# Optimization experiments

Hardware: AMD Instinct MI355X
Metric: run time of the kernel (lower is better)

## Reference

```python
import jax, jax.numpy as jnp
import numpy as np

B, S, DIM = 1, 2048, 4096
N_HEADS, N_KV_HEADS = 32, 8
HEAD_DIM = DIM // N_HEADS            # 128
N_REP = N_HEADS // N_KV_HEADS        # 4
Q_SIZE = N_HEADS * HEAD_DIM          # 4096
KV_SIZE = N_KV_HEADS * HEAD_DIM      # 1024


def setup_inputs() -> dict:
    key = jax.random.key(0)
    ks = jax.random.split(key, 5)
    x = jax.random.normal(ks[0], (B, S, DIM), dtype=jnp.float32)
    # RoPE tables: freqs_cis[s, j] = exp(i * s * theta_j), theta_j = 10000^(-2j/head_dim)
    theta = 10000.0 ** (-jnp.arange(0, HEAD_DIM, 2, dtype=jnp.float32) / HEAD_DIM)
    ang = jnp.arange(S, dtype=jnp.float32)[:, None] * theta[None, :]  # [S, HEAD_DIM//2]
    freqs_cos = jnp.cos(ang)
    freqs_sin = jnp.sin(ang)
    # causal additive mask [1,1,S,S]
    causal = jnp.tril(jnp.ones((S, S), dtype=bool))
    mask = jnp.where(causal, 0.0, -1e9).astype(jnp.float32)[None, None]
    wqkv = jax.random.normal(ks[1], (Q_SIZE + 2 * KV_SIZE, DIM), dtype=jnp.float32) * (DIM ** -0.5)
    wo = jax.random.normal(ks[2], (DIM, Q_SIZE), dtype=jnp.float32) * (Q_SIZE ** -0.5)
    return {"x": x, "freqs_cos": freqs_cos, "freqs_sin": freqs_sin, "mask": mask,
            "wqkv": wqkv, "wo": wo}


def _apply_rope(t, cos, sin):
    # t: [B, S, H, D]; cos/sin: [S, D//2]  (complex multiply on (even, odd) pairs)
    b, s, h, d = t.shape
    tp = t.reshape(b, s, h, d // 2, 2)
    t0, t1 = tp[..., 0], tp[..., 1]
    c = cos[None, :, None, :]
    sn = sin[None, :, None, :]
    out = jnp.stack([t0 * c - t1 * sn, t0 * sn + t1 * c], axis=-1)
    return out.reshape(b, s, h, d)


def reference(x, freqs_cos, freqs_sin, mask, wqkv, wo):
    bsz, seqlen, _ = x.shape
    qkv = jnp.einsum('bsd,od->bso', x, wqkv)  # fused QKV projection
    xq = qkv[..., :Q_SIZE].reshape(bsz, seqlen, N_HEADS, HEAD_DIM)
    xk = qkv[..., Q_SIZE:Q_SIZE + KV_SIZE].reshape(bsz, seqlen, N_KV_HEADS, HEAD_DIM)
    xv = qkv[..., Q_SIZE + KV_SIZE:].reshape(bsz, seqlen, N_KV_HEADS, HEAD_DIM)
    # rotary embedding on q, k
    xq = _apply_rope(xq, freqs_cos, freqs_sin)
    xk = _apply_rope(xk, freqs_cos, freqs_sin)
    # cache insertion (prefill: cache == current k/v), layout [B, KVH, S, D]
    cache_k = jnp.swapaxes(xk, 1, 2)
    cache_v = jnp.swapaxes(xv, 1, 2)
    # GQA repeat_kv -> [B, H, S, D]
    keys = jnp.repeat(cache_k, N_REP, axis=1)
    values = jnp.repeat(cache_v, N_REP, axis=1)
    # scores: einsum 'ijkl,ikml->ikjm' with xq [b,s,h,d], keys [b,h,t,d] -> [b,h,s,t]
    scores = jnp.einsum('bshd,bhtd->bhst', xq, keys) / jnp.sqrt(jnp.float32(HEAD_DIM))
    scores = scores + mask
    scores = jax.nn.softmax(scores.astype(jnp.float32), axis=-1).astype(xq.dtype)
    out = jnp.einsum('bhst,bhtd->bhsd', scores, values)  # [B, H, S, D]
    out = jnp.swapaxes(out, 1, 2).reshape(bsz, seqlen, Q_SIZE)
    return jnp.einsum('bso,do->bsd', out, wo)
```

## Files before the change

### kernel.cpp

```cpp
#include <hip/hip_runtime.h>
#include <hip/hip_bf16.h>
#include <cstdint>
#include <cstddef>


typedef __attribute__((ext_vector_type(4)))  float    f32x4;
typedef __attribute__((ext_vector_type(16))) float    f32x16;
typedef __attribute__((ext_vector_type(8)))  __bf16   bf16x8;
typedef __attribute__((ext_vector_type(4)))  __bf16   bf16x4;
typedef __attribute__((ext_vector_type(2)))  __bf16   bf16x2;
typedef __attribute__((ext_vector_type(4)))  uint32_t u32x4;

typedef const __attribute__((address_space(1))) void* gaddr_t;
typedef __attribute__((address_space(3))) void*       laddr_t;

#define S_LEN   2048
#define DIM_    4096
#define NHEADS  32
#define NKV     8
#define HD      128
#define QKV_LD  6144
#define KOFF    4096
#define VOFF    5120

#define EXP2F(x) __builtin_amdgcn_exp2f(x)

__global__ void cvt_f32_bf16(const float* __restrict__ in, __bf16* __restrict__ out, int n4) {
  int idx = blockIdx.x * blockDim.x + threadIdx.x;
  int stride = gridDim.x * blockDim.x;
  for (int i = idx; i < n4; i += stride) {
    float4 v = reinterpret_cast<const float4*>(in)[i];
    bf16x4 o;
    o[0] = (__bf16)v.x; o[1] = (__bf16)v.y; o[2] = (__bf16)v.z; o[3] = (__bf16)v.w;
    reinterpret_cast<bf16x4*>(out)[i] = o;
  }
}

__global__ void rope_kernel(__bf16* __restrict__ qkv, const float* __restrict__ fc,
                            const float* __restrict__ fs) {
  int tid = blockIdx.x * 256 + threadIdx.x;
  int i = tid & 63;
  int t = tid >> 6;
  int h = t % 40;
  int s = t / 40;
  int col = (h < NHEADS) ? (h * HD + 2 * i) : (KOFF + (h - NHEADS) * HD + 2 * i);
  size_t off = (size_t)s * QKV_LD + col;
  float c = fc[s * 64 + i], sn = fs[s * 64 + i];
  bf16x2 v = *reinterpret_cast<bf16x2*>(&qkv[off]);
  float t0 = (float)v[0], t1 = (float)v[1];
  bf16x2 o;
  o[0] = (__bf16)(t0 * c - t1 * sn);
  o[1] = (__bf16)(t0 * sn + t1 * c);
  *reinterpret_cast<bf16x2*>(&qkv[off]) = o;
}

__device__ __forceinline__ void stg64(const __bf16* __restrict__ P, int ld, int row0,
                                      int kt, char* dst, int tid) {
  int r = tid >> 3, g = tid & 7;
  int row = row0 + r;
  const __bf16* src = P + (size_t)row * ld + kt * 64 + ((g ^ (row & 7)) * 8);
  __builtin_amdgcn_global_load_lds((gaddr_t)src,
      (laddr_t)(dst + (tid & ~63) * 16), 16, 0, 0);
}

template <int QM, int QN, bool RA, bool RB, int VW>
__device__ __forceinline__ void g1_phase(const __bf16* __restrict__ Ab,
                                         const __bf16* __restrict__ Bb,
                                         f32x4 (&acc)[8][4],
                                         bf16x8 (&afr)[4][2], bf16x8 (&bfr)[2][2],
                                         int wm, int wn, int l15, int hi, int tid,
                                         const __bf16* __restrict__ SP, int sld,
                                         int srow, int skt, char* sdst, bool doSt) {
  if constexpr (RA) {
#pragma unroll
    for (int fm = 0; fm < 4; ++fm) {
      int R = wm * 128 + QM * 64 + fm * 16 + l15;
#pragma unroll
      for (int kk = 0; kk < 2; ++kk)
        afr[fm][kk] = *reinterpret_cast<const bf16x8*>(
            (const char*)Ab + R * 128 + (((kk * 4 + hi) ^ (R & 7)) * 16));
    }
  }
  if constexpr (RB) {
#pragma unroll
    for (int fn = 0; fn < 2; ++fn) {
      int R = wn * 64 + QN * 32 + fn * 16 + l15;
#pragma unroll
      for (int kk = 0; kk < 2; ++kk)
        bfr[fn][kk] = *reinterpret_cast<const bf16x8*>(
            (const char*)Bb + R * 128 + (((kk * 4 + hi) ^ (R & 7)) * 16));
    }
  }
  if (doSt) {
    stg64(SP, sld, srow, skt, sdst, tid);
    stg64(SP, sld, srow + 64, skt, sdst + 8192, tid);
  }
  __builtin_amdgcn_s_barrier();
  asm volatile("s_waitcnt lgkmcnt(0)" ::: "memory");
  __builtin_amdgcn_sched_barrier(0);
  __builtin_amdgcn_s_setprio(1);
#pragma unroll
  for (int kk = 0; kk < 2; ++kk)
#pragma unroll
    for (int fm = 0; fm < 4; ++fm)
#pragma unroll
      for (int fn = 0; fn < 2; ++fn)
        acc[QM * 4 + fm][QN * 2 + fn] = __builtin_amdgcn_mfma_f32_16x16x32_bf16(
            afr[fm][kk], bfr[fn][kk], acc[QM * 4 + fm][QN * 2 + fn], 0, 0, 0);
  __builtin_amdgcn_s_setprio(0);
  if constexpr (VW == 4) asm volatile("s_waitcnt vmcnt(4)" ::: "memory");
  if constexpr (VW == 0) asm volatile("s_waitcnt vmcnt(0)" ::: "memory");
  __builtin_amdgcn_s_barrier();
}

__global__ __launch_bounds__(512) void g1_8p(const __bf16* __restrict__ A,
                                             const __bf16* __restrict__ B,
                                             __bf16* __restrict__ C, int K,
                                             int lda, int ldb, int ldc) {
  __shared__ __align__(16) __bf16 As[2][256 * 64];
  __shared__ __align__(16) __bf16 Bs[2][256 * 64];
  const int tid = threadIdx.x;
  const int l15 = tid & 15, hi = (tid >> 4) & 3, w = tid >> 6;
  const int wm = w >> 2, wn = w & 3;
  const int bid = blockIdx.x, xcd = bid & 7, lid = bid >> 3;
  const int m0 = (lid % 8) * 256;
  const int n0 = (xcd * 3 + lid / 8) * 256;

  f32x4 acc[8][4] = {};
  bf16x8 afr[4][2], bfr[2][2];
  char* A0 = (char*)As[0]; char* A1 = (char*)As[1];
  char* B0 = (char*)Bs[0]; char* B1 = (char*)Bs[1];

  stg64(A, lda, m0,       0, A0,         tid); stg64(A, lda, m0 + 64,  0, A0 + 8192,  tid);
  stg64(B, ldb, n0,       0, B0,         tid); stg64(B, ldb, n0 + 64,  0, B0 + 8192,  tid);
  stg64(A, lda, m0 + 128, 0, A0 + 16384, tid); stg64(A, lda, m0 + 192, 0, A0 + 24576, tid);
  stg64(B, ldb, n0 + 128, 0, B0 + 16384, tid); stg64(B, ldb, n0 + 192, 0, B0 + 24576, tid);
  stg64(A, lda, m0,       1, A1,         tid); stg64(A, lda, m0 + 64,  1, A1 + 8192,  tid);
  stg64(B, ldb, n0 + 128, 1, B1 + 16384, tid); stg64(B, ldb, n0 + 192, 1, B1 + 24576, tid);
  asm volatile("s_waitcnt vmcnt(4)" ::: "memory");
  __builtin_amdgcn_s_barrier();

  const int nt = K >> 6;
  for (int it = 0; it < nt; it += 2) {
    const bool sB = (it + 2 < nt), sC = (it + 3 < nt);
    const bool last = !sB;
    const __bf16* Ab0 = As[0]; const __bf16* Bb0 = Bs[0];
    const __bf16* Ab1 = As[1]; const __bf16* Bb1 = Bs[1];
    g1_phase<0, 0, true,  true, -1>(Ab0, Bb0, acc, afr, bfr, wm, wn, l15, hi, tid,
                                    A, lda, m0 + 128, it + 1, A1 + 16384, true);
    g1_phase<0, 1, false, true, -1>(Ab0, Bb0, acc, afr, bfr, wm, wn, l15, hi, tid,
                                    B, ldb, n0, it + 1, B1, true);
    g1_phase<1, 1, true, false, -1>(Ab0, Bb0, acc, afr, bfr, wm, wn, l15, hi, tid,
                                    A, lda, m0, it + 2, A0, sB);
    if (last)
      g1_phase<1, 0, false, true, 0>(Ab0, Bb0, acc, afr, bfr, wm, wn, l15, hi, tid,
                                     B, ldb, n0 + 128, it + 2, B0 + 16384, sB);
    else
      g1_phase<1, 0, false, true, 4>(Ab0, Bb0, acc, afr, bfr, wm, wn, l15, hi, tid,
                                     B, ldb, n0 + 128, it + 2, B0 + 16384, sB);
    g1_phase<0, 0, true,  true, -1>(Ab1, Bb1, acc, afr, bfr, wm, wn, l15, hi, tid,
                                    A, lda, m0 + 128, it + 2, A0 + 16384, sB);
    g1_phase<0, 1, false, true, -1>(Ab1, Bb1, acc, afr, bfr, wm, wn, l15, hi, tid,
                                    B, ldb, n0, it + 2, B0, sB);
    g1_phase<1, 1, true, false, -1>(Ab1, Bb1, acc, afr, bfr, wm, wn, l15, hi, tid,
                                    A, lda, m0, it + 3, A1, sC);
    if (last)
      g1_phase<1, 0, false, true, 0>(Ab1, Bb1, acc, afr, bfr, wm, wn, l15, hi, tid,
                                     B, ldb, n0 + 128, it + 3, B1 + 16384, sC);
    else
      g1_phase<1, 0, false, true, 4>(Ab1, Bb1, acc, afr, bfr, wm, wn, l15, hi, tid,
                                     B, ldb, n0 + 128, it + 3, B1 + 16384, sC);
  }

#pragma unroll
  for (int qm = 0; qm < 2; ++qm)
#pragma unroll
    for (int fm = 0; fm < 4; ++fm)
#pragma unroll
      for (int qn = 0; qn < 2; ++qn)
#pragma unroll
        for (int fn = 0; fn < 2; ++fn)
#pragma unroll
          for (int j = 0; j < 4; ++j) {
            int row = m0 + wm * 128 + qm * 64 + fm * 16 + hi * 4 + j;
            int col = n0 + wn * 64 + qn * 32 + fn * 16 + l15;
            C[(size_t)row * ldc + col] = (__bf16)acc[qm * 4 + fm][qn * 2 + fn][j];
          }
}

template <int MW, int NW, int KH, int NST, bool VM>
__device__ __forceinline__ void phase32(const __bf16* __restrict__ Ab,
                                        const __bf16* __restrict__ Bb,
                                        f32x16 (&acc)[MW][NW],
                                        int wm, int wn, int l31, int hi, int tid,
                                        const __bf16* __restrict__ SP, int sld,
                                        int srow0, char* sdst, int kt, bool st) {
  bf16x8 af[MW][2], bfr[NW][2];
#pragma unroll
  for (int mi = 0; mi < MW; ++mi) {
    int R = wm * (MW * 32) + mi * 32 + l31;
#pragma unroll
    for (int k2 = 0; k2 < 2; ++k2)
      af[mi][k2] = *reinterpret_cast<const bf16x8*>(
          (const char*)Ab + R * 128 + (((KH * 4 + k2 * 2 + hi) ^ (R & 7)) * 16));
  }
#pragma unroll
  for (int ni = 0; ni < NW; ++ni) {
    int R = wn * (NW * 32) + ni * 32 + l31;
#pragma unroll
    for (int k2 = 0; k2 < 2; ++k2)
      bfr[ni][k2] = *reinterpret_cast<const bf16x8*>(
          (const char*)Bb + R * 128 + (((KH * 4 + k2 * 2 + hi) ^ (R & 7)) * 16));
  }
  if (st) {
#pragma unroll
    for (int h = 0; h < NST; ++h)
      stg64(SP, sld, srow0 + h * 64, kt, sdst + h * 8192, tid);
  }
  __builtin_amdgcn_s_barrier();
  asm volatile("s_waitcnt lgkmcnt(0)" ::: "memory");
  __builtin_amdgcn_sched_barrier(0);
  __builtin_amdgcn_s_setprio(1);
#pragma unroll
  for (int k2 = 0; k2 < 2; ++k2)
#pragma unroll
    for (int mi = 0; mi < MW; ++mi)
#pragma unroll
      for (int ni = 0; ni < NW; ++ni)
        acc[mi][ni] = __builtin_amdgcn_mfma_f32_32x32x16_bf16(af[mi][k2], bfr[ni][k2],
                                                              acc[mi][ni], 0, 0, 0);
  __builtin_amdgcn_s_setprio(0);
  if (VM) asm volatile("s_waitcnt vmcnt(0)" ::: "memory");
  __builtin_amdgcn_s_barrier();
}

template <int BM, int BN, int MB, int NPX, typename OutT>
__global__ __launch_bounds__(512) void gemm32(const __bf16* __restrict__ A,
                                              const __bf16* __restrict__ B,
                                              OutT* __restrict__ C, int K,
                                              int lda, int ldb, int ldc) {
  constexpr int MW = BM / 64;
  constexpr int NW = BN / 128;
  constexpr int AST = BM / 64, BST = BN / 64;
  __shared__ __align__(16) __bf16 As[2][BM * 64];
  __shared__ __align__(16) __bf16 Bs[2][BN * 64];
  const int tid = threadIdx.x;
  const int lane = tid & 63, l31 = lane & 31, hi = lane >> 5, w = tid >> 6;
  const int wm = w >> 2, wn = w & 3;
  const int bid = blockIdx.x, xcd = bid & 7, lid = bid >> 3;
  const int m0 = (lid % MB) * BM;
  const int n0 = (xcd * NPX + lid / MB) * BN;

  f32x16 acc[MW][NW] = {};

#pragma unroll
  for (int h = 0; h < AST; ++h) stg64(A, lda, m0 + h * 64, 0, (char*)As[0] + h * 8192, tid);
#pragma unroll
  for (int h = 0; h < BST; ++h) stg64(B, ldb, n0 + h * 64, 0, (char*)Bs[0] + h * 8192, tid);
  asm volatile("s_waitcnt vmcnt(0)" ::: "memory");
  __builtin_amdgcn_s_barrier();

  const int ntiles = K >> 6;
  for (int t = 0; t < ntiles; ++t) {
    const int cur = t & 1;
    const __bf16* Ab = As[cur];
    const __bf16* Bb = Bs[cur];
    char* dA = (char*)As[1 - cur];
    char* dB = (char*)Bs[1 - cur];
    const bool st = (t + 1 < ntiles);
    phase32<MW, NW, 0, AST, false>(Ab, Bb, acc, wm, wn, l31, hi, tid,
                                   A, lda, m0, dA, t + 1, st);
    phase32<MW, NW, 1, BST, true >(Ab, Bb, acc, wm, wn, l31, hi, tid,
                                   B, ldb, n0, dB, t + 1, st);
  }

#pragma unroll
  for (int mi = 0; mi < MW; ++mi)
#pragma unroll
    for (int ni = 0; ni < NW; ++ni)
#pragma unroll
      for (int e = 0; e < 16; ++e) {
        int row = m0 + wm * (MW * 32) + mi * 32 + (e & 3) + 8 * (e >> 2) + 4 * hi;
        int col = n0 + wn * (NW * 32) + ni * 32 + l31;
        C[(size_t)row * ldc + col] = (OutT)acc[mi][ni][e];
      }
}

__device__ inline uint32_t pack2(float a, float b) {
  bf16x2 t; t[0] = (__bf16)a; t[1] = (__bf16)b;
  return __builtin_bit_cast(uint32_t, t);
}

__global__ __launch_bounds__(256, 2) void attn_kernel(const __bf16* __restrict__ qkv,
                                                      __bf16* __restrict__ out) {
  __shared__ __align__(16) __bf16 Ks[2][64 * 128];
  __shared__ __align__(16) __bf16 Vt[2][128][66];
  const int tid = threadIdx.x;
  const int lane = tid & 63, l31 = lane & 31, hi = lane >> 5, wq = tid >> 6;
  const int head = blockIdx.x & 31;
  const int g = blockIdx.x >> 5;
  const int qt = (g < 8) ? (15 - g) : (g - 8);
  const int q0 = qt * 128;
  const int nt = 2 * qt + 2;
  const int kvh = head >> 2;
  const float sc2 = 0.08838834764831845f * 1.44269504089f;
  const int qr = q0 + wq * 32 + l31;

  bf16x8 vr[2][2];

  auto stage_k = [&](int tt, int buf) {
#pragma unroll
    for (int i = 0; i < 4; ++i) {
      int c = i * 256 + tid;
      int r = c >> 4, gg = c & 15;
      const __bf16* gk = qkv + (size_t)(tt * 64 + r) * QKV_LD + KOFF + kvh * HD + ((gg ^ (r & 7)) * 8);
      __builtin_amdgcn_global_load_lds((gaddr_t)gk,
          (laddr_t)((char*)Ks[buf] + (tid & ~63) * 16 + i * 4096), 16, 0, 0);
    }
  };
  auto load_v = [&](int tt) {
#pragma unroll
    for (int i = 0; i < 2; ++i) {
      int task = i * 256 + tid;
      int p = task >> 4, cg = task & 15;
      const __bf16* vp = qkv + (size_t)(tt * 64 + 2 * p) * QKV_LD + VOFF + kvh * HD + cg * 8;
      vr[i][0] = *reinterpret_cast<const bf16x8*>(vp);
      vr[i][1] = *reinterpret_cast<const bf16x8*>(vp + QKV_LD);
    }
  };
  auto write_v = [&](int buf) {
#pragma unroll
    for (int i = 0; i < 2; ++i) {
      int task = i * 256 + tid;
      int p = task >> 4, cg = task & 15;
#pragma unroll
      for (int e = 0; e < 8; ++e) {
        bf16x2 pkv; pkv[0] = vr[i][0][e]; pkv[1] = vr[i][1][e];
        *reinterpret_cast<bf16x2*>(&Vt[buf][cg * 8 + e][2 * p]) = pkv;
      }
    }
  };

  bf16x8 qf[8];
  {
    const __bf16* qp = qkv + (size_t)qr * QKV_LD + head * HD + hi * 8;
#pragma unroll
    for (int ks = 0; ks < 8; ++ks) qf[ks] = *reinterpret_cast<const bf16x8*>(qp + ks * 16);
  }
  f32x16 o[4] = {};
  float m_run = -3e38f, l_run = 0.f;

  stage_k(0, 0); load_v(0); write_v(0);

  for (int t = 0; t < nt; ++t) {
    const int cur = t & 1;
    __syncthreads();
    if (t + 1 < nt) { stage_k(t + 1, 1 - cur); load_v(t + 1); }

    f32x16 st[2];
#pragma unroll
    for (int sub = 0; sub < 2; ++sub) {
      f32x16 acc = {};
      int r = sub * 32 + l31;
#pragma unroll
      for (int ks = 0; ks < 8; ++ks) {
        int gg = (ks * 2 + hi) ^ (r & 7);
        bf16x8 kf = *reinterpret_cast<const bf16x8*>((char*)Ks[cur] + r * 256 + gg * 16);
        acc = __builtin_amdgcn_mfma_f32_32x32x16_bf16(kf, qf[ks], acc, 0, 0, 0);
      }
      st[sub] = acc;
    }
    if (t >= nt - 2) {
      const int kv0 = t * 64;
#pragma unroll
      for (int sub = 0; sub < 2; ++sub)
#pragma unroll
        for (int e = 0; e < 16; ++e) {
          int kvg = kv0 + sub * 32 + (e & 3) + 8 * (e >> 2) + 4 * hi;
          if (kvg > qr) st[sub][e] = -1e30f;
        }
    }
    float pm = st[0][0];
#pragma unroll
    for (int e = 1; e < 16; ++e) pm = fmaxf(pm, st[0][e]);
#pragma unroll
    for (int e = 0; e < 16; ++e) pm = fmaxf(pm, st[1][e]);
    pm = fmaxf(pm, __shfl_xor(pm, 32));
    pm *= sc2;
    if (!__all(pm - m_run <= 8.f)) {
      float mn = fmaxf(m_run, pm);
      float fsc = EXP2F(m_run - mn);
      m_run = mn;
      l_run *= fsc;
#pragma unroll
      for (int dt = 0; dt < 4; ++dt)
#pragma unroll
        for (int e = 0; e < 16; ++e) o[dt][e] *= fsc;
    }
    float rs = 0.f;
#pragma unroll
    for (int sub = 0; sub < 2; ++sub)
#pragma unroll
      for (int e = 0; e < 16; ++e) {
        float p = EXP2F(__builtin_fmaf(st[sub][e], sc2, -m_run));
        st[sub][e] = p;
        rs += p;
      }
    rs += __shfl_xor(rs, 32);
    l_run += rs;

    uint32_t pk[16];
#pragma unroll
    for (int sub = 0; sub < 2; ++sub)
#pragma unroll
      for (int i = 0; i < 8; ++i)
        pk[sub * 8 + i] = pack2(st[sub][2 * i], st[sub][2 * i + 1]);
    uint32_t rv[8];
#pragma unroll
    for (int m = 0; m < 8; ++m) {
      int base = 4 * (m >> 1) + (m & 1);
      uint32_t snd = hi ? pk[base] : pk[base + 2];
      rv[m] = __shfl_xor(snd, 32);
    }
    bf16x8 pf[4];
#pragma unroll
    for (int tt = 0; tt < 4; ++tt) {
      u32x4 wv;
      wv[0] = hi ? rv[2 * tt]     : pk[4 * tt];
      wv[1] = hi ? rv[2 * tt + 1] : pk[4 * tt + 1];
      wv[2] = hi ? pk[4 * tt + 2] : rv[2 * tt];
      wv[3] = hi ? pk[4 * tt + 3] : rv[2 * tt + 1];
      pf[tt] = __builtin_bit_cast(bf16x8, wv);
    }
#pragma unroll
    for (int dt = 0; dt < 4; ++dt) {
      int dr = dt * 32 + l31;
#pragma unroll
      for (int tt = 0; tt < 4; ++tt) {
        bf16x8 vf = *reinterpret_cast<const bf16x8*>((char*)&Vt[cur][0][0] + dr * 132 + tt * 32 + hi * 16);
        o[dt] = __builtin_amdgcn_mfma_f32_32x32x16_bf16(vf, pf[tt], o[dt], 0, 0, 0);
      }
    }
    if (t + 1 < nt) write_v(1 - cur);
  }

  float inv = 1.f / l_run;
  __bf16* scr = &Ks[0][0] + wq * 1280;
  const int qq = lane >> 1, part = lane & 1;
#pragma unroll
  for (int dt = 0; dt < 4; ++dt) {
    __syncthreads();
#pragma unroll
    for (int i = 0; i < 8; ++i) {
      int d0 = (2 * i & 3) + 8 * (i >> 1) + 4 * hi;
      bf16x2 prr;
      prr[0] = (__bf16)(o[dt][2 * i] * inv);
      prr[1] = (__bf16)(o[dt][2 * i + 1] * inv);
      *reinterpret_cast<bf16x2*>(scr + l31 * 40 + d0) = prr;
    }
    __syncthreads();
    bf16x8 r0 = *reinterpret_cast<const bf16x8*>(scr + qq * 40 + part * 16);
    bf16x8 r1 = *reinterpret_cast<const bf16x8*>(scr + qq * 40 + part * 16 + 8);
    __bf16* op = out + (size_t)(q0 + wq * 32 + qq) * DIM_ + head * HD + dt * 32 + part * 16;
    *reinterpret_cast<bf16x8*>(op) = r0;
    *reinterpret_cast<bf16x8*>(op + 8) = r1;
  }
}

extern "C" void kernel_launch(void* const* d_in, const int* in_sizes, int n_in,
                              void* d_out, int out_size, void* d_ws, size_t ws_size,
                              hipStream_t stream) {
  (void)in_sizes; (void)n_in; (void)out_size; (void)ws_size;
  const float* x    = (const float*)d_in[0];
  const float* fc   = (const float*)d_in[1];
  const float* fs   = (const float*)d_in[2];
  const float* wqkv = (const float*)d_in[4];
  const float* wo   = (const float*)d_in[5];
  float* out = (float*)d_out;

  char* ws = (char*)d_ws;
  __bf16* xb    = (__bf16*)(ws);
  __bf16* wqkvb = (__bf16*)(ws + 16777216);
  __bf16* wob   = (__bf16*)(ws + 67108864);
  __bf16* qkv   = (__bf16*)(ws + 100663296);
  __bf16* attnO = xb;

  cvt_f32_bf16<<<2048, 256, 0, stream>>>(x,    xb,    (S_LEN * DIM_) / 4);
  cvt_f32_bf16<<<2048, 256, 0, stream>>>(wqkv, wqkvb, (6144 * DIM_) / 4);
  cvt_f32_bf16<<<2048, 256, 0, stream>>>(wo,   wob,   (DIM_ * DIM_) / 4);

  g1_8p<<<192, 512, 0, stream>>>(xb, wqkvb, qkv, DIM_, DIM_, DIM_, QKV_LD);

  rope_kernel<<<(S_LEN * 40 * 64) / 256, 256, 0, stream>>>(qkv, fc, fs);

  attn_kernel<<<512, 256, 0, stream>>>(qkv, attnO);

  gemm32<128, 256, 16, 2, float><<<256, 512, 0, stream>>>(attnO, wob, out, DIM_, DIM_, DIM_, DIM_);
}
```

Before: 327.5 us.

## Fuse RoPE into QKV GEMM epilogue, merge conversions, prioritize attention MFMAs

Three conversion kernels become one launch, and the standalone RoPE kernel is removed by applying the rotation in the QKV GEMM epilogue: lane pairs swap values with a shuffle and read cos/sin per row. The attention kernel also raises wave priority around its two MFMA blocks. This removes two kernel launches and a full read-modify-write pass over Q/K. In exchange the GEMM store path gains extra global loads of the frequency tables and shuffles.

Result: slower. 342.3 us (+4.5%).

```diff
diff --git a/kernel.cpp b/kernel.cpp
--- a/kernel.cpp
+++ b/kernel.cpp
@@ -25,33 +25,24 @@
 
 #define EXP2F(x) __builtin_amdgcn_exp2f(x)
 
-__global__ void cvt_f32_bf16(const float* __restrict__ in, __bf16* __restrict__ out, int n4) {
+#define N4_X  2097152
+#define N4_W  6291456
+#define N4_O  4194304
+__global__ void cvt3(const float* __restrict__ x, __bf16* __restrict__ xb,
+                     const float* __restrict__ wq, __bf16* __restrict__ wqb,
+                     const float* __restrict__ wo, __bf16* __restrict__ wob) {
   int idx = blockIdx.x * blockDim.x + threadIdx.x;
   int stride = gridDim.x * blockDim.x;
-  for (int i = idx; i < n4; i += stride) {
-    float4 v = reinterpret_cast<const float4*>(in)[i];
+  for (int i = idx; i < N4_X + N4_W + N4_O; i += stride) {
+    const float* src; __bf16* dst; int k;
+    if (i < N4_X)            { src = x;  dst = xb;  k = i; }
+    else if (i < N4_X + N4_W){ src = wq; dst = wqb; k = i - N4_X; }
+    else                     { src = wo; dst = wob; k = i - N4_X - N4_W; }
+    float4 v = reinterpret_cast<const float4*>(src)[k];
     bf16x4 o;
     o[0] = (__bf16)v.x; o[1] = (__bf16)v.y; o[2] = (__bf16)v.z; o[3] = (__bf16)v.w;
-    reinterpret_cast<bf16x4*>(out)[i] = o;
-  }
-}
-
-__global__ void rope_kernel(__bf16* __restrict__ qkv, const float* __restrict__ fc,
-                            const float* __restrict__ fs) {
-  int tid = blockIdx.x * 256 + threadIdx.x;
-  int i = tid & 63;
-  int t = tid >> 6;
-  int h = t % 40;
-  int s = t / 40;
-  int col = (h < NHEADS) ? (h * HD + 2 * i) : (KOFF + (h - NHEADS) * HD + 2 * i);
-  size_t off = (size_t)s * QKV_LD + col;
-  float c = fc[s * 64 + i], sn = fs[s * 64 + i];
-  bf16x2 v = *reinterpret_cast<bf16x2*>(&qkv[off]);
-  float t0 = (float)v[0], t1 = (float)v[1];
-  bf16x2 o;
-  o[0] = (__bf16)(t0 * c - t1 * sn);
-  o[1] = (__bf16)(t0 * sn + t1 * c);
-  *reinterpret_cast<bf16x2*>(&qkv[off]) = o;
+    reinterpret_cast<bf16x4*>(dst)[k] = o;
+  }
 }
 
 __device__ __forceinline__ void stg64(const __bf16* __restrict__ P, int ld, int row0,
@@ -115,8 +106,10 @@
 
 __global__ __launch_bounds__(512) void g1_8p(const __bf16* __restrict__ A,
                                              const __bf16* __restrict__ B,
-                                             __bf16* __restrict__ C, int K,
-                                             int lda, int ldb, int ldc) {
+                                             __bf16* __restrict__ C,
+                                             const float* __restrict__ fc,
+                                             const float* __restrict__ fs,
+                                             int K, int lda, int ldb, int ldc) {
   __shared__ __align__(16) __bf16 As[2][256 * 64];
   __shared__ __align__(16) __bf16 Bs[2][256 * 64];
   const int tid = threadIdx.x;
@@ -172,6 +165,8 @@
                                      B, ldb, n0 + 128, it + 3, B1 + 16384, sC);
   }
 
+  const bool isqk = (n0 < VOFF);
+  const float sgn = (l15 & 1) ? 1.f : -1.f;
 #pragma unroll
   for (int qm = 0; qm < 2; ++qm)
 #pragma unroll
@@ -179,13 +174,21 @@
 #pragma unroll
       for (int qn = 0; qn < 2; ++qn)
 #pragma unroll
-        for (int fn = 0; fn < 2; ++fn)
+        for (int fn = 0; fn < 2; ++fn) {
+          int col = n0 + wn * 64 + qn * 32 + fn * 16 + l15;
+          int fi = (col & 127) >> 1;
 #pragma unroll
           for (int j = 0; j < 4; ++j) {
             int row = m0 + wm * 128 + qm * 64 + fm * 16 + hi * 4 + j;
-            int col = n0 + wn * 64 + qn * 32 + fn * 16 + l15;
-            C[(size_t)row * ldc + col] = (__bf16)acc[qm * 4 + fm][qn * 2 + fn][j];
+            float v = acc[qm * 4 + fm][qn * 2 + fn][j];
+            if (isqk) {
+              float p = __shfl_xor(v, 1);
+              float c = fc[row * 64 + fi], sn = fs[row * 64 + fi];
+              v = v * c + sgn * p * sn;
+            }
+            C[(size_t)row * ldc + col] = (__bf16)v;
           }
+        }
 }
 
 template <int MW, int NW, int KH, int NST, bool VM>
@@ -358,6 +361,7 @@
     if (t + 1 < nt) { stage_k(t + 1, 1 - cur); load_v(t + 1); }
 
     f32x16 st[2];
+    __builtin_amdgcn_s_setprio(1);
 #pragma unroll
     for (int sub = 0; sub < 2; ++sub) {
       f32x16 acc = {};
@@ -370,6 +374,7 @@
       }
       st[sub] = acc;
     }
+    __builtin_amdgcn_s_setprio(0);
     if (t >= nt - 2) {
       const int kv0 = t * 64;
 #pragma unroll
@@ -432,6 +437,7 @@
       wv[3] = hi ? pk[4 * tt + 3] : rv[2 * tt + 1];
       pf[tt] = __builtin_bit_cast(bf16x8, wv);
     }
+    __builtin_amdgcn_s_setprio(1);
 #pragma unroll
     for (int dt = 0; dt < 4; ++dt) {
       int dr = dt * 32 + l31;
@@ -441,6 +447,7 @@
         o[dt] = __builtin_amdgcn_mfma_f32_32x32x16_bf16(vf, pf[tt], o[dt], 0, 0, 0);
       }
     }
+    __builtin_amdgcn_s_setprio(0);
     if (t + 1 < nt) write_v(1 - cur);
   }
 
@@ -485,13 +492,9 @@
   __bf16* qkv   = (__bf16*)(ws + 100663296);
   __bf16* attnO = xb;
 
-  cvt_f32_bf16<<<2048, 256, 0, stream>>>(x,    xb,    (S_LEN * DIM_) / 4);
-  cvt_f32_bf16<<<2048, 256, 0, stream>>>(wqkv, wqkvb, (6144 * DIM_) / 4);
-  cvt_f32_bf16<<<2048, 256, 0, stream>>>(wo,   wob,   (DIM_ * DIM_) / 4);
-
-  g1_8p<<<192, 512, 0, stream>>>(xb, wqkvb, qkv, DIM_, DIM_, DIM_, QKV_LD);
-
-  rope_kernel<<<(S_LEN * 40 * 64) / 256, 256, 0, stream>>>(qkv, fc, fs);
+  cvt3<<<2048, 256, 0, stream>>>(x, xb, wqkv, wqkvb, wo, wob);
+
+  g1_8p<<<192, 512, 0, stream>>>(xb, wqkvb, qkv, fc, fs, DIM_, DIM_, DIM_, QKV_LD);
 
   attn_kernel<<<512, 256, 0, stream>>>(qkv, attnO);
 
```
